# Performance work log

Measured on AMD Instinct MI355X. Metric: run time of the kernel, lower is better.

## Reference

```python
import jax, jax.numpy as jnp
from jax import lax
import numpy as np

B, NR, NC, FEAT = 8, 1024, 1024, 768
N = NR + NC
HID, GATD, GRUD = 256, 128, 64
NEG = -9e15  # matches -9000000000000000.0 in torch source


def setup_inputs() -> dict:
    key = jax.random.key(0)
    ks = jax.random.split(key, 24)
    s = 0.02
    nrm = lambda k, shp: jax.random.normal(k, shp, jnp.float32) * s
    z = lambda shp: jnp.zeros(shp, jnp.float32)
    inp = {}
    inp['req_nodes'] = jax.random.normal(ks[0], (B, NR, FEAT), jnp.float32)
    inp['code_nodes'] = jax.random.normal(ks[1], (B, NC, FEAT), jnp.float32)
    inp['alignment_matrix'] = jax.random.bernoulli(ks[2], 0.05, (B, N, N)).astype(jnp.float32)
    inp['total_nodes'] = jax.random.randint(ks[3], (B,), N // 2, N + 1).astype(jnp.int32)
    # feature_projection
    inp['W_proj'] = nrm(ks[4], (HID, FEAT)); inp['b_proj'] = z((HID,))
    # GAT layer 1 (HID->HID), attention weight a is Linear(2*HID, 1, bias=False)
    inp['W_g1'] = nrm(ks[5], (HID, HID)); inp['b_g1'] = z((HID,)); inp['a_g1'] = nrm(ks[6], (2 * HID,))
    # GAT layer 2 (HID->GATD)
    inp['W_g2'] = nrm(ks[7], (GATD, HID)); inp['b_g2'] = z((GATD,)); inp['a_g2'] = nrm(ks[8], (2 * GATD,))
    # bidirectional GRU (torch layout: [3H, in], gates r|z|n)
    inp['Wih_f'] = nrm(ks[9], (3 * GRUD, GATD)); inp['Whh_f'] = nrm(ks[10], (3 * GRUD, GRUD))
    inp['bih_f'] = z((3 * GRUD,)); inp['bhh_f'] = z((3 * GRUD,))
    inp['Wih_b'] = nrm(ks[11], (3 * GRUD, GATD)); inp['Whh_b'] = nrm(ks[12], (3 * GRUD, GRUD))
    inp['bih_b'] = z((3 * GRUD,)); inp['bhh_b'] = z((3 * GRUD,))
    inp['W_fus'] = nrm(ks[13], (GRUD, 2 * GRUD)); inp['b_fus'] = z((GRUD,))
    inp['W_c1'] = nrm(ks[14], (HID // 2, GRUD)); inp['b_c1'] = z((HID // 2,))
    inp['W_c2'] = nrm(ks[15], (1, HID // 2)); inp['b_c2'] = z((1,))
    return inp


def _gat_layer(x, adj, mask, W, b, a):
    # h: [B, N, D]
    h = x @ W.T + b
    D = h.shape[-1]
    # attention(concat(h_i, h_j)) == a[:D]@h_i + a[D:]@h_j -> never materialize [B,N,N,2D]
    s_src = h @ a[:D]   # [B, N]
    s_dst = h @ a[D:]   # [B, N]
    e = jax.nn.leaky_relu(s_src[:, :, None] + s_dst[:, None, :], 0.01)  # [B,N,N]
    att = jax.nn.softmax(jnp.where(adj > 0, e, NEG), axis=-1)
    out = jnp.einsum('bij,bjd->bid', att, h)
    return out * mask[..., None]


def _gru_dir(xproj, Whh, bhh, reverse):
    # xproj: [B, T, 3H] = x @ Wih.T + bih (precomputed)
    Bv, H = xproj.shape[0], Whh.shape[1]
    def step(h, xt):
        gh = h @ Whh.T + bhh
        ir, iz, inn = jnp.split(xt, 3, axis=-1)
        hr, hz, hn = jnp.split(gh, 3, axis=-1)
        r = jax.nn.sigmoid(ir + hr)
        zt = jax.nn.sigmoid(iz + hz)
        n = jnp.tanh(inn + r * hn)
        hnew = (1.0 - zt) * n + zt * h
        return hnew, hnew
    h0 = jnp.zeros((Bv, H), xproj.dtype)
    _, ys = lax.scan(step, h0, jnp.swapaxes(xproj, 0, 1), reverse=reverse)
    return jnp.swapaxes(ys, 0, 1)  # [B, T, H]


def _forward(req_nodes, code_nodes, alignment_matrix, total_nodes,
             W_proj, b_proj, W_g1, b_g1, a_g1, W_g2, b_g2, a_g2,
             Wih_f, Whh_f, bih_f, bhh_f, Wih_b, Whh_b, bih_b, bhh_b,
             W_fus, b_fus, W_c1, b_c1, W_c2, b_c2):
    x = jnp.concatenate([req_nodes, code_nodes], axis=1)        # [B, N, FEAT]
    proj = jax.nn.relu(x @ W_proj.T + b_proj)                   # dropout is eval-mode identity
    Nt = proj.shape[1]
    mask = (jnp.arange(Nt)[None, :] < total_nodes[:, None]).astype(proj.dtype)  # [B, N]
    g1 = _gat_layer(proj, alignment_matrix, mask, W_g1, b_g1, a_g1)
    g1 = jax.nn.relu(g1) * mask[..., None]
    gat_out = _gat_layer(g1, alignment_matrix, mask, W_g2, b_g2, a_g2)
    gat_out = gat_out * mask[..., None]  # extra masking as in torch source (idempotent)
    gf = _gru_dir(gat_out @ Wih_f.T + bih_f, Whh_f, bhh_f, reverse=False)
    gb = _gru_dir(gat_out @ Wih_b.T + bih_b, Whh_b, bhh_b, reverse=True)
    gru_out = jnp.concatenate([gf, gb], axis=-1) * mask[..., None]  # [B, N, 2*GRUD]
    fused = gru_out @ W_fus.T + b_fus                               # [B, N, GRUD]
    pooled = jnp.mean(fused, axis=1)  # AdaptiveAvgPool1d(1) over seq dim
    h1 = jax.nn.relu(pooled @ W_c1.T + b_c1)
    out = jax.nn.sigmoid(h1 @ W_c2.T + b_c2)  # [B, 1]
    return out


def reference(req_nodes, code_nodes, alignment_matrix, total_nodes,
              W_proj, b_proj, W_g1, b_g1, a_g1, W_g2, b_g2, a_g2,
              Wih_f, Whh_f, bih_f, bhh_f, Wih_b, Whh_b, bih_b, bhh_b,
              W_fus, b_fus, W_c1, b_c1, W_c2, b_c2):
    return _forward(req_nodes, code_nodes, alignment_matrix, total_nodes,
                    W_proj, b_proj, W_g1, b_g1, a_g1, W_g2, b_g2, a_g2,
                    Wih_f, Whh_f, bih_f, bhh_f, Wih_b, Whh_b, bih_b, bhh_b,
                    W_fus, b_fus, W_c1, b_c1, W_c2, b_c2)
```

## Files before the change

### kernel.cpp

```cpp
#include <hip/hip_runtime.h>
#include <stdint.h>

#define EMAX 256

typedef short bf16x8 __attribute__((ext_vector_type(8)));
typedef float f32x4 __attribute__((ext_vector_type(4)));
typedef _Float16 h2_t __attribute__((ext_vector_type(2)));

#define SWZ(r, c) ((r) * 64 + ((c) ^ (((r) & 7) << 3)))

__device__ __forceinline__ uint16_t f2bf(float f) {
    union { float f; uint32_t u; } v; v.f = f;
    uint32_t u = v.u;
    uint32_t r = (u + 0x7FFFu + ((u >> 16) & 1u)) >> 16;
    return (uint16_t)r;
}
__device__ __forceinline__ float bf2f(uint16_t h) {
    union { uint32_t u; float f; } v; v.u = ((uint32_t)h) << 16;
    return v.f;
}
__device__ __forceinline__ h2_t u2h2(uint32_t u) {
    union { uint32_t u; h2_t h; } v; v.u = u;
    return v.h;
}
__device__ __forceinline__ uint32_t cvtpk_bf16(float lo, float hi) {
    uint32_t d;
    asm("v_cvt_pk_bf16_f32 %0, %1, %2" : "=v"(d) : "v"(lo), "v"(hi));
    return d;
}

__global__ __launch_bounds__(256) void k_prep(const float* wp, const float* wg1, const float* wg2,
                                              const float* wif, const float* wib,
                                              const float* whf, const float* whb,
                                              const float* bihf, const float* bihb,
                                              uint16_t* op, uint16_t* og1, uint16_t* og2,
                                              uint16_t* oifb, _Float16* ohf, _Float16* ohb, float* bihfb,
                                              float* __restrict__ Sz) {
    int i = blockIdx.x * 256 + threadIdx.x;
    if (i < 196608) op[i]  = f2bf(wp[i]);
    if (i < 65536)  og1[i] = f2bf(wg1[i]);
    if (i < 32768)  og2[i] = f2bf(wg2[i]);
    if (i < 24576)  { oifb[i] = f2bf(wif[i]); oifb[24576 + i] = f2bf(wib[i]); }
    if (i < 12288)  { ohf[i] = (_Float16)whf[i]; ohb[i] = (_Float16)whb[i]; }
    if (i < 192)    { bihfb[i] = bihf[i]; bihfb[192 + i] = bihb[i]; }
    if (i < 1024)   Sz[i] = 0.f;
}

__global__ __launch_bounds__(256) void k_g1e(const float* __restrict__ req, const float* __restrict__ code,
                                             const uint16_t* __restrict__ Bw,
                                             const float* __restrict__ bias,
                                             uint16_t* __restrict__ C,
                                             const float* __restrict__ adj,
                                             uint16_t* __restrict__ eidx, int* __restrict__ ecnt) {
    __shared__ __align__(16) uint16_t As[64 * 64];
    __shared__ __align__(16) uint16_t Bs[64 * 64];
    int tid = threadIdx.x;
    if (blockIdx.x < 4096) {
        int row  = blockIdx.x * 4 + (tid >> 6);
        int lane = tid & 63;
        const float4* ar4 = (const float4*)(adj + (size_t)row * 2048) + lane;
        float4 vv[8];
#pragma unroll
        for (int c = 0; c < 8; ++c) vv[c] = ar4[c * 64];
        uint32_t m4[8]; int c4[8];
#pragma unroll
        for (int c = 0; c < 8; ++c) {
            uint32_t m = (vv[c].x > 0.f ? 1u : 0u) | (vv[c].y > 0.f ? 2u : 0u)
                       | (vv[c].z > 0.f ? 4u : 0u) | (vv[c].w > 0.f ? 8u : 0u);
            m4[c] = m; c4[c] = __popc(m);
        }
        int pk[4];
#pragma unroll
        for (int q = 0; q < 4; ++q) pk[q] = c4[2 * q] | (c4[2 * q + 1] << 16);
#pragma unroll
        for (int off = 1; off < 64; off <<= 1) {
#pragma unroll
            for (int q = 0; q < 4; ++q) {
                int o = __shfl_up(pk[q], off);
                if (lane >= off) pk[q] += o;
            }
        }
        uint16_t* outr = eidx + (size_t)row * EMAX;
        int base = 0;
#pragma unroll
        for (int c = 0; c < 8; ++c) {
            int incl = (pk[c >> 1] >> ((c & 1) * 16)) & 0xffff;
            int Tc   = __shfl(incl, 63);
            int p    = base + incl - c4[c];
            uint32_t mm = m4[c];
            int cb = c * 256 + lane * 4;
            while (mm) {
                int k = __builtin_ctz(mm);
                mm &= mm - 1u;
                if (p < EMAX) outr[p] = (uint16_t)(cb + k);
                ++p;
            }
            base += Tc;
        }
        if (lane == 0) ecnt[row] = (base < EMAX) ? base : EMAX;
        return;
    }
    constexpr int K = 768, N = 256;
    int g = blockIdx.x - 4096;
    int n0 = (g & 3) * 64, m0 = (g >> 2) * 64;
    int wave = tid >> 6, lane = tid & 63;
    int quad = lane >> 4, l16 = lane & 15;
    f32x4 acc[4] = {};
    int ar = tid >> 3;
    int ac = (tid & 7) * 8;
    const float4* rowp[2];
#pragma unroll
    for (int h = 0; h < 2; ++h) {
        int n = m0 + ar + h * 32;
        int b = n >> 11, n2 = n & 2047;
        const float* s = (n2 < 1024) ? (req  + ((size_t)(b * 1024 + n2)) * 768)
                                     : (code + ((size_t)(b * 1024 + (n2 - 1024))) * 768);
        rowp[h] = (const float4*)s + (ac >> 2);
    }
    for (int kb = 0; kb < K; kb += 64) {
#pragma unroll
        for (int h = 0; h < 2; ++h) {
            float4 f0 = rowp[h][(kb >> 2) + 0];
            float4 f1 = rowp[h][(kb >> 2) + 1];
            uint4 pk;
            pk.x = cvtpk_bf16(f0.x, f0.y); pk.y = cvtpk_bf16(f0.z, f0.w);
            pk.z = cvtpk_bf16(f1.x, f1.y); pk.w = cvtpk_bf16(f1.z, f1.w);
            *(uint4*)&As[SWZ(ar + h * 32, ac)] = pk;
        }
        *(uint4*)&Bs[SWZ(ar, ac)]      = *(const uint4*)(Bw + (size_t)(n0 + ar)      * K + kb + ac);
        *(uint4*)&Bs[SWZ(ar + 32, ac)] = *(const uint4*)(Bw + (size_t)(n0 + ar + 32) * K + kb + ac);
        __syncthreads();
#pragma unroll
        for (int kk = 0; kk < 64; kk += 32) {
            bf16x8 af = *(bf16x8*)&As[SWZ(wave * 16 + l16, kk + quad * 8)];
#pragma unroll
            for (int c = 0; c < 4; ++c) {
                bf16x8 bfr = *(bf16x8*)&Bs[SWZ(c * 16 + l16, kk + quad * 8)];
                acc[c] = __builtin_amdgcn_mfma_f32_16x16x32_bf16(af, bfr, acc[c], 0, 0, 0);
            }
        }
        __syncthreads();
    }
#pragma unroll
    for (int c = 0; c < 4; ++c) {
        int col = n0 + c * 16 + l16;
        float bv = bias[col];
#pragma unroll
        for (int rg = 0; rg < 4; ++rg) {
            int row = m0 + wave * 16 + quad * 4 + rg;
            float v = fmaxf(acc[c][rg] + bv, 0.f);
            C[(size_t)row * N + col] = f2bf(v);
        }
    }
}

template<int ACT, int MODE>
__global__ __launch_bounds__(256) void k_gemm(const uint16_t* __restrict__ A,
                                              const uint16_t* __restrict__ Bw,
                                              const float* __restrict__ bias,
                                              void* __restrict__ Cv, void* __restrict__ Cv2,
                                              int M, int N, int K) {
    __shared__ __align__(16) uint16_t As[64 * 64];
    __shared__ __align__(16) uint16_t Bs[64 * 64];
    int tid = threadIdx.x;
    int n0 = blockIdx.x * 64, m0 = blockIdx.y * 64;
    int wave = tid >> 6, lane = tid & 63;
    int quad = lane >> 4, l16 = lane & 15;
    f32x4 acc[4] = {};
    int ar = tid >> 3;
    int ac = (tid & 7) * 8;
    for (int kb = 0; kb < K; kb += 64) {
        *(uint4*)&As[SWZ(ar, ac)]      = *(const uint4*)(A  + (size_t)(m0 + ar)      * K + kb + ac);
        *(uint4*)&As[SWZ(ar + 32, ac)] = *(const uint4*)(A  + (size_t)(m0 + ar + 32) * K + kb + ac);
        *(uint4*)&Bs[SWZ(ar, ac)]      = *(const uint4*)(Bw + (size_t)(n0 + ar)      * K + kb + ac);
        *(uint4*)&Bs[SWZ(ar + 32, ac)] = *(const uint4*)(Bw + (size_t)(n0 + ar + 32) * K + kb + ac);
        __syncthreads();
#pragma unroll
        for (int kk = 0; kk < 64; kk += 32) {
            bf16x8 af = *(bf16x8*)&As[SWZ(wave * 16 + l16, kk + quad * 8)];
#pragma unroll
            for (int c = 0; c < 4; ++c) {
                bf16x8 bfr = *(bf16x8*)&Bs[SWZ(c * 16 + l16, kk + quad * 8)];
                acc[c] = __builtin_amdgcn_mfma_f32_16x16x32_bf16(af, bfr, acc[c], 0, 0, 0);
            }
        }
        __syncthreads();
    }
#pragma unroll
    for (int c = 0; c < 4; ++c) {
        int col = n0 + c * 16 + l16;
        float bv = bias ? bias[col] : 0.f;
#pragma unroll
        for (int rg = 0; rg < 4; ++rg) {
            int row = m0 + wave * 16 + quad * 4 + rg;
            float v = acc[c][rg] + bv;
            if (ACT == 1) v = fmaxf(v, 0.f);
            if (MODE == 1)      ((uint16_t*)Cv)[(size_t)row * N + col] = f2bf(v);
            else if (MODE == 0) ((float*)Cv)[(size_t)row * N + col] = v;
            else {
                int tc = (col < 192) ? col : col - 192;
                int dc = (tc & 63) * 4 + (tc >> 6);
                float* dst = (col < 192) ? (float*)Cv : (float*)Cv2;
                dst[(size_t)row * 256 + dc] = v;
            }
        }
    }
}

template<int D>
__global__ __launch_bounds__(256) void k_attvec(const uint16_t* __restrict__ H,
                                                const float* __restrict__ a,
                                                float* __restrict__ ssrc,
                                                float* __restrict__ sdst) {
    int row  = blockIdx.x * 4 + (threadIdx.x >> 6);
    int lane = threadIdx.x & 63;
    constexpr int PER = D >> 6;
    const uint32_t* hr = (const uint32_t*)(H + (size_t)row * D + lane * PER);
    float s0 = 0.f, s1 = 0.f;
#pragma unroll
    for (int q = 0; q < PER / 2; ++q) {
        uint32_t hv = hr[q];
        int d = lane * PER + q * 2;
        float h0 = bf2f((uint16_t)hv), h1 = bf2f((uint16_t)(hv >> 16));
        s0 += h0 * a[d] + h1 * a[d + 1];
        s1 += h0 * a[D + d] + h1 * a[D + d + 1];
    }
    for (int off = 32; off; off >>= 1) { s0 += __shfl_down(s0, off); s1 += __shfl_down(s1, off); }
    if (lane == 0) { ssrc[row] = s0; sdst[row] = s1; }
}

#define ACC4(hv, wv) { \
    a0 = fmaf(wv, bf2f((uint16_t)(hv).x), a0); \
    a1 = fmaf(wv, bf2f((uint16_t)((hv).x >> 16)), a1); \
    a2 = fmaf(wv, bf2f((uint16_t)(hv).y), a2); \
    a3 = fmaf(wv, bf2f((uint16_t)((hv).y >> 16)), a3); }

template<int D, int LAYER1>
__global__ __launch_bounds__(256) void k_agg(const uint16_t* __restrict__ H,
                                             const float* __restrict__ ssrc,
                                             const float* __restrict__ sdst,
                                             const uint16_t* __restrict__ eidx,
                                             const int* __restrict__ ecnt,
                                             const int* __restrict__ total,
                                             uint16_t* __restrict__ out) {
    constexpr int LPG = (D == 256) ? 64 : 32;
    constexpr int G   = 64 / LPG;
    constexpr int RS  = D / 4;
    __shared__ __align__(16) uint2 ew[4][EMAX];
    int tid  = threadIdx.x;
    int wid  = tid >> 6, lane = tid & 63;
    int grp  = lane / LPG;
    int c    = lane % LPG;
    int b    = blockIdx.x & 7;
    int i    = ((blockIdx.x >> 3) << 2) + wid;
    int row  = (b << 11) + i;
    uint2* orow = (uint2*)(out + (size_t)row * D);
    if (i >= total[b]) {
        if (grp == 0) { uint2 z; z.x = 0u; z.y = 0u; orow[c] = z; }
        return;
    }
    int cnt = ecnt[row];
    const uint2* H2 = (const uint2*)(H + (size_t)b * 2048 * D);
    float a0 = 0.f, a1 = 0.f, a2 = 0.f, a3 = 0.f;
    if (cnt > 0) {
        float sv = ssrc[row];
        const uint16_t* er = eidx + (size_t)row * EMAX;
        int   jj[4]; float ee[4];
#pragma unroll
        for (int k = 0; k < 4; ++k) {
            int t = lane + 64 * k;
            int j = (t < cnt) ? (int)er[t] : 0;
            float x = sv + sdst[b * 2048 + j];
            float e = (x > 0.f) ? x : 0.01f * x;
            if (t >= cnt) e = -1e30f;
            jj[k] = j; ee[k] = e;
        }
        float m = fmaxf(fmaxf(ee[0], ee[1]), fmaxf(ee[2], ee[3]));
#pragma unroll
        for (int off = 32; off; off >>= 1) m = fmaxf(m, __shfl_xor(m, off));
        float w[4]; float s = 0.f;
#pragma unroll
        for (int k = 0; k < 4; ++k) { w[k] = __expf(ee[k] - m); s += w[k]; }
#pragma unroll
        for (int off = 32; off; off >>= 1) s += __shfl_xor(s, off);
        float inv = 1.f / s;
#pragma unroll
        for (int k = 0; k < 4; ++k) {
            uint2 p; p.x = (uint32_t)jj[k]; p.y = __float_as_uint(w[k] * inv);
            ew[wid][lane + 64 * k] = p;
        }
        asm volatile("s_waitcnt lgkmcnt(0)" ::: "memory");
        constexpr int EPB = 4 * G;
        int cntP = (cnt + EPB - 1) & ~(EPB - 1);
        if constexpr (G == 1) {
            for (int t = 0; t < cntP; t += 4) {
                uint2 e0 = ew[wid][t + 0], e1 = ew[wid][t + 1];
                uint2 e2 = ew[wid][t + 2], e3 = ew[wid][t + 3];
                uint2 h0 = H2[(size_t)e0.x * RS + c];
                uint2 h1 = H2[(size_t)e1.x * RS + c];
                uint2 h2 = H2[(size_t)e2.x * RS + c];
                uint2 h3 = H2[(size_t)e3.x * RS + c];
                ACC4(h0, __uint_as_float(e0.y));
                ACC4(h1, __uint_as_float(e1.y));
                ACC4(h2, __uint_as_float(e2.y));
                ACC4(h3, __uint_as_float(e3.y));
            }
        } else {
            for (int t = 0; t < cntP; t += 8) {
                uint2 e0 = ew[wid][t + 0 + grp], e1 = ew[wid][t + 2 + grp];
                uint2 e2 = ew[wid][t + 4 + grp], e3 = ew[wid][t + 6 + grp];
                uint2 h0 = H2[(size_t)e0.x * RS + c];
                uint2 h1 = H2[(size_t)e1.x * RS + c];
                uint2 h2 = H2[(size_t)e2.x * RS + c];
                uint2 h3 = H2[(size_t)e3.x * RS + c];
                ACC4(h0, __uint_as_float(e0.y));
                ACC4(h1, __uint_as_float(e1.y));
                ACC4(h2, __uint_as_float(e2.y));
                ACC4(h3, __uint_as_float(e3.y));
            }
        }
    } else {
        for (int t = grp; t < 2048; t += G) {
            uint2 hv = H2[(size_t)t * RS + c];
            ACC4(hv, 1.f);
        }
        a0 *= (1.f / 2048.f); a1 *= (1.f / 2048.f);
        a2 *= (1.f / 2048.f); a3 *= (1.f / 2048.f);
    }
    if constexpr (G == 2) {
        a0 += __shfl_xor(a0, 32); a1 += __shfl_xor(a1, 32);
        a2 += __shfl_xor(a2, 32); a3 += __shfl_xor(a3, 32);
    }
    if (LAYER1) {
        a0 = fmaxf(a0, 0.f); a1 = fmaxf(a1, 0.f);
        a2 = fmaxf(a2, 0.f); a3 = fmaxf(a3, 0.f);
    }
    if (grp == 0) {
        uint2 pk;
        pk.x = (uint32_t)f2bf(a0) | ((uint32_t)f2bf(a1) << 16);
        pk.y = (uint32_t)f2bf(a2) | ((uint32_t)f2bf(a3) << 16);
        orow[c] = pk;
    }
}

#define CHUNKS 16
#define CLEN   128
#define WARM   64
#define FDOT2(acc, p, wq) acc = __builtin_amdgcn_fdot2(p, u2h2(wq), acc, false)
#define DOTBLK(hq, q) { \
    h2_t p0 = u2h2(hq.x), p1 = u2h2(hq.y), p2 = u2h2(hq.z), p3 = u2h2(hq.w); \
    FDOT2(ar0, p0, wr[4*q+0]); FDOT2(ar1, p1, wr[4*q+1]); FDOT2(ar2, p2, wr[4*q+2]); FDOT2(ar3, p3, wr[4*q+3]); \
    FDOT2(az0, p0, wz[4*q+0]); FDOT2(az1, p1, wz[4*q+1]); FDOT2(az2, p2, wz[4*q+2]); FDOT2(az3, p3, wz[4*q+3]); \
    FDOT2(an0, p0, wn[4*q+0]); FDOT2(an1, p1, wn[4*q+1]); FDOT2(an2, p2, wn[4*q+2]); FDOT2(an3, p3, wn[4*q+3]); }
#define GRU_STEP(xq) { \
    uint4 h0 = hv4[0], h1 = hv4[1], h2v = hv4[2], h3 = hv4[3]; \
    uint4 h4 = hv4[4], h5 = hv4[5], h6 = hv4[6], h7 = hv4[7]; \
    float ar0 = br, ar1 = 0.f, ar2 = 0.f, ar3 = 0.f; \
    float az0 = bz, az1 = 0.f, az2 = 0.f, az3 = 0.f; \
    float an0 = bn, an1 = 0.f, an2 = 0.f, an3 = 0.f; \
    DOTBLK(h0, 0) DOTBLK(h1, 1) DOTBLK(h2v, 2) DOTBLK(h3, 3) \
    DOTBLK(h4, 4) DOTBLK(h5, 5) DOTBLK(h6, 6) DOTBLK(h7, 7) \
    float ghr = (ar0 + ar1) + (ar2 + ar3); \
    float ghz = (az0 + az1) + (az2 + az3); \
    float ghn = (an0 + an1) + (an2 + an3); \
    float er = __expf(-(xq.x + ghr)); \
    float r = __builtin_amdgcn_rcpf(1.f + er); \
    float ez = __expf(-(xq.y + ghz)); \
    float z = __builtin_amdgcn_rcpf(1.f + ez); \
    float nv = fmaf(r, ghn, xq.z); \
    float en = __expf(-2.f * nv); \
    float n = fmaf(-2.f, __builtin_amdgcn_rcpf(1.f + en), 1.f); \
    hj = fmaf(z, hj - n, n); \
    sj += (t < Tcur) ? hj : 0.f; \
    hb[j] = (_Float16)hj; \
    asm volatile("" ::: "memory"); \
    t += dt; }

__global__ __attribute__((amdgpu_flat_work_group_size(64, 64), amdgpu_waves_per_eu(1, 1)))
void k_gru(const float* __restrict__ XPf, const float* __restrict__ XPb,
           const _Float16* __restrict__ WhF, const _Float16* __restrict__ WhB,
           const float* __restrict__ bhh_f, const float* __restrict__ bhh_b,
           const int* __restrict__ total,
           float* __restrict__ S) {
    int blk   = blockIdx.x;
    int chunk = blk & (CHUNKS - 1);
    int sc    = blk >> 4;
    int dir   = sc >> 3;
    int b     = sc & 7;
    int j     = threadIdx.x;
    const float* XP  = dir ? XPb : XPf;
    const uint32_t* Wd = (const uint32_t*)(dir ? WhB : WhF);
    const float* bhh = dir ? bhh_b : bhh_f;
    uint32_t wr[32], wz[32], wn[32];
#pragma unroll
    for (int c = 0; c < 32; ++c) {
        wr[c] = Wd[(size_t)(      j) * 32 + c];
        wz[c] = Wd[(size_t)( 64 + j) * 32 + c];
        wn[c] = Wd[(size_t)(128 + j) * 32 + c];
    }
    float br = bhh[j], bz = bhh[64 + j], bn = bhh[128 + j];
    __shared__ __align__(16) _Float16 hbuf[64];
    _Float16* hb = hbuf;
    hb[j] = (_Float16)0.f;
    asm volatile("s_waitcnt lgkmcnt(0)" ::: "memory");
    float hj = 0.f, sj = 0.f;
    int Tb = total[b];
    int s0 = chunk * CLEN - WARM;
    int W0 = WARM;
    if (s0 < 0) { s0 = 0; W0 = 0; }
    const float4* xbase = (const float4*)(XP + (size_t)b * 2048 * 256) + j;
    int xstep = dir ? -64 : 64;
    const float4* xptr = xbase + (size_t)(dir ? (2047 - s0) : s0) * 64;
    float4 x0 = *xptr; xptr += xstep;
    float4 x1 = *xptr; xptr += xstep;
    float4 x2 = *xptr; xptr += xstep;
    float4 x3 = *xptr; xptr += xstep;
    int t = dir ? (2047 - s0) : s0, dt = dir ? -1 : 1;
    const uint4* hv4 = (const uint4*)hb;
    int Tcur = -1;
    for (int su = 0; su < W0; su += 4) {
        GRU_STEP(x0) x0 = *xptr; xptr += xstep;
        GRU_STEP(x1) x1 = *xptr; xptr += xstep;
        GRU_STEP(x2) x2 = *xptr; xptr += xstep;
        GRU_STEP(x3) x3 = *xptr; xptr += xstep;
    }
    Tcur = Tb;
    for (int su = 0; su < CLEN; su += 4) {
        GRU_STEP(x0) x0 = *xptr; xptr += xstep;
        GRU_STEP(x1) x1 = *xptr; xptr += xstep;
        GRU_STEP(x2) x2 = *xptr; xptr += xstep;
        GRU_STEP(x3) x3 = *xptr; xptr += xstep;
    }
    atomicAdd(&S[b * 128 + dir * 64 + j], sj);
}

__global__ __launch_bounds__(128) void k_final(const float* __restrict__ S,
                                               const float* __restrict__ Wfus, const float* __restrict__ bfus,
                                               const float* __restrict__ Wc1, const float* __restrict__ bc1,
                                               const float* __restrict__ Wc2, const float* __restrict__ bc2,
                                               float* __restrict__ out) {
    __shared__ float pool[64];
    __shared__ float red[128];
    int tid = threadIdx.x;
    for (int b = 0; b < 8; ++b) {
        if (tid < 64) {
            float a = 0.f;
            for (int jj = 0; jj < 128; ++jj) a += S[b * 128 + jj] * Wfus[tid * 128 + jj];
            pool[tid] = bfus[tid] + a * (1.f / 2048.f);
        }
        __syncthreads();
        float a1 = 0.f;
        for (int d = 0; d < 64; ++d) a1 += pool[d] * Wc1[tid * 64 + d];
        float h = fmaxf(a1 + bc1[tid], 0.f);
        red[tid] = h * Wc2[tid];
        __syncthreads();
        for (int s = 64; s; s >>= 1) { if (tid < s) red[tid] += red[tid + s]; __syncthreads(); }
        if (tid == 0) out[b] = 1.f / (1.f + __expf(-(red[0] + bc2[0])));
        __syncthreads();
    }
}

extern "C" void kernel_launch(void* const* d_in, const int* in_sizes, int n_in,
                              void* d_out, int out_size, void* d_ws, size_t ws_size,
                              hipStream_t stream) {
    (void)in_sizes; (void)n_in; (void)out_size; (void)ws_size;
    const float* req   = (const float*)d_in[0];
    const float* code  = (const float*)d_in[1];
    const float* adj   = (const float*)d_in[2];
    const int*   total = (const int*)  d_in[3];
    const float* W_proj = (const float*)d_in[4];
    const float* b_proj = (const float*)d_in[5];
    const float* W_g1   = (const float*)d_in[6];
    const float* b_g1   = (const float*)d_in[7];
    const float* a_g1   = (const float*)d_in[8];
    const float* W_g2   = (const float*)d_in[9];
    const float* b_g2   = (const float*)d_in[10];
    const float* a_g2   = (const float*)d_in[11];
    const float* Wih_f  = (const float*)d_in[12];
    const float* Whh_f  = (const float*)d_in[13];
    const float* bih_f  = (const float*)d_in[14];
    const float* bhh_f  = (const float*)d_in[15];
    const float* Wih_b  = (const float*)d_in[16];
    const float* Whh_b  = (const float*)d_in[17];
    const float* bih_b  = (const float*)d_in[18];
    const float* bhh_b  = (const float*)d_in[19];
    const float* W_fus  = (const float*)d_in[20];
    const float* b_fus  = (const float*)d_in[21];
    const float* W_c1   = (const float*)d_in[22];
    const float* b_c1   = (const float*)d_in[23];
    const float* W_c2   = (const float*)d_in[24];
    const float* b_c2   = (const float*)d_in[25];

    char* ws = (char*)d_ws;
    float*    XPf  = (float*)(ws + 4096);
    float*    XPb  = (float*)(ws + 4096 + 16777216 + 4096);
    uint16_t* EIDX = (uint16_t*)(ws + 25169920);
    uint16_t* WPb  = (uint16_t*)(ws + 33570816);
    uint16_t* WG1b = (uint16_t*)(ws + 33964032);
    uint16_t* WG2b = (uint16_t*)(ws + 34095104);
    uint16_t* WIFB = (uint16_t*)(ws + 34160640);
    uint16_t* Pbf  = (uint16_t*)(ws + 34262016);
    uint16_t* H1bf = (uint16_t*)(ws + 42650624);
    uint16_t* H2bf = (uint16_t*)(ws + 42650624);
    uint16_t* G2bf = (uint16_t*)(ws + 46844928);
    uint16_t* G1bf = (uint16_t*)(ws + 51039232);
    int*      ECNT = (int*)     (ws + 59427840);
    float* s1src = (float*)(ws + 59493376);
    float* s1dst = (float*)(ws + 59558912);
    float* s2src = (float*)(ws + 59624448);
    float* s2dst = (float*)(ws + 59689984);
    float* Sbuf  = (float*)(ws + 59755520);
    _Float16* WhFh = (_Float16*)(ws + 59759616);
    _Float16* WhBh = (_Float16*)(ws + 59784192);
    float* BIHFB   = (float*)(ws + 59808768);

    k_prep<<<768, 256, 0, stream>>>(W_proj, W_g1, W_g2, Wih_f, Wih_b, Whh_f, Whh_b, bih_f, bih_b,
                                    WPb, WG1b, WG2b, WIFB, WhFh, WhBh, BIHFB, Sbuf);

    k_g1e<<<5120, 256, 0, stream>>>(req, code, WPb, b_proj, Pbf, adj, EIDX, ECNT);

    k_gemm<0, 1><<<dim3(4, 256), 256, 0, stream>>>(Pbf, WG1b, b_g1, H1bf, nullptr, 16384, 256, 256);
    k_attvec<256><<<4096, 256, 0, stream>>>(H1bf, a_g1, s1src, s1dst);
    k_agg<256, 1><<<4096, 256, 0, stream>>>(H1bf, s1src, s1dst, EIDX, ECNT, total, G1bf);

    k_gemm<0, 1><<<dim3(2, 256), 256, 0, stream>>>(G1bf, WG2b, b_g2, H2bf, nullptr, 16384, 128, 256);
    k_attvec<128><<<4096, 256, 0, stream>>>(H2bf, a_g2, s2src, s2dst);
    k_agg<128, 0><<<4096, 256, 0, stream>>>(H2bf, s2src, s2dst, EIDX, ECNT, total, G2bf);

    k_gemm<0, 2><<<dim3(6, 256), 256, 0, stream>>>(G2bf, WIFB, BIHFB, XPf, XPb, 16384, 384, 128);

    k_gru<<<256, 64, 0, stream>>>(XPf, XPb, WhFh, WhBh, bhh_f, bhh_b, total, Sbuf);

    k_final<<<1, 128, 0, stream>>>(Sbuf, W_fus, b_fus, W_c1, b_c1, W_c2, b_c2, (float*)d_out);
}
```

Baseline: 538.5 us.

## Process multiple adjacency rows per wave with double-buffered loads in edge extraction

The edge-list extraction part of the fused kernel now launches 512 blocks instead of 4096. Each wave handles 8 adjacency rows strided by 2048, loading the next row into a second register buffer while compacting the current one. This is meant to overlap global-memory latency with the scan work and cut block launch overhead. It raises register pressure and lowers the number of waves in flight for the memory-bound scan.

```diff
diff --git a/kernel.cpp b/kernel.cpp
--- a/kernel.cpp
+++ b/kernel.cpp
@@ -55,53 +55,54 @@
     __shared__ __align__(16) uint16_t As[64 * 64];
     __shared__ __align__(16) uint16_t Bs[64 * 64];
     int tid = threadIdx.x;
-    if (blockIdx.x < 4096) {
-        int row  = blockIdx.x * 4 + (tid >> 6);
-        int lane = tid & 63;
-        const float4* ar4 = (const float4*)(adj + (size_t)row * 2048) + lane;
-        float4 vv[8];
-#pragma unroll
-        for (int c = 0; c < 8; ++c) vv[c] = ar4[c * 64];
-        uint32_t m4[8]; int c4[8];
-#pragma unroll
-        for (int c = 0; c < 8; ++c) {
-            uint32_t m = (vv[c].x > 0.f ? 1u : 0u) | (vv[c].y > 0.f ? 2u : 0u)
-                       | (vv[c].z > 0.f ? 4u : 0u) | (vv[c].w > 0.f ? 8u : 0u);
-            m4[c] = m; c4[c] = __popc(m);
-        }
-        int pk[4];
-#pragma unroll
-        for (int q = 0; q < 4; ++q) pk[q] = c4[2 * q] | (c4[2 * q + 1] << 16);
-#pragma unroll
-        for (int off = 1; off < 64; off <<= 1) {
-#pragma unroll
-            for (int q = 0; q < 4; ++q) {
-                int o = __shfl_up(pk[q], off);
-                if (lane >= off) pk[q] += o;
-            }
-        }
-        uint16_t* outr = eidx + (size_t)row * EMAX;
-        int base = 0;
-#pragma unroll
-        for (int c = 0; c < 8; ++c) {
-            int incl = (pk[c >> 1] >> ((c & 1) * 16)) & 0xffff;
-            int Tc   = __shfl(incl, 63);
-            int p    = base + incl - c4[c];
-            uint32_t mm = m4[c];
-            int cb = c * 256 + lane * 4;
-            while (mm) {
-                int k = __builtin_ctz(mm);
-                mm &= mm - 1u;
-                if (p < EMAX) outr[p] = (uint16_t)(cb + k);
-                ++p;
-            }
-            base += Tc;
-        }
-        if (lane == 0) ecnt[row] = (base < EMAX) ? base : EMAX;
+    if (blockIdx.x < 512) {
+        int wid  = tid >> 6, lane = tid & 63;
+        int gw   = blockIdx.x * 4 + wid;
+        const float4* base = (const float4*)adj + lane;
+        float4 va[8], vb[8];
+#define LOADROW(dst, r) { const float4* p_ = base + (size_t)(r) * 512; \
+        _Pragma("unroll") for (int c_ = 0; c_ < 8; ++c_) dst[c_] = p_[c_ * 64]; }
+#define PROCROW(src, r) { \
+        uint32_t m4[8]; int c4[8]; \
+        _Pragma("unroll") for (int c_ = 0; c_ < 8; ++c_) { \
+            uint32_t m_ = (src[c_].x > 0.f ? 1u : 0u) | (src[c_].y > 0.f ? 2u : 0u) \
+                        | (src[c_].z > 0.f ? 4u : 0u) | (src[c_].w > 0.f ? 8u : 0u); \
+            m4[c_] = m_; c4[c_] = __popc(m_); } \
+        int pk[4]; \
+        _Pragma("unroll") for (int q_ = 0; q_ < 4; ++q_) pk[q_] = c4[2*q_] | (c4[2*q_+1] << 16); \
+        _Pragma("unroll") for (int off_ = 1; off_ < 64; off_ <<= 1) { \
+            _Pragma("unroll") for (int q_ = 0; q_ < 4; ++q_) { \
+                int o_ = __shfl_up(pk[q_], off_); \
+                if (lane >= off_) pk[q_] += o_; } } \
+        uint16_t* outr = eidx + (size_t)(r) * EMAX; \
+        int bse = 0; \
+        _Pragma("unroll") for (int c_ = 0; c_ < 8; ++c_) { \
+            int incl = (pk[c_ >> 1] >> ((c_ & 1) * 16)) & 0xffff; \
+            int Tc_  = __shfl(incl, 63); \
+            int p_   = bse + incl - c4[c_]; \
+            uint32_t mm = m4[c_]; \
+            int cb = c_ * 256 + lane * 4; \
+            while (mm) { int k_ = __builtin_ctz(mm); mm &= mm - 1u; \
+                if (p_ < EMAX) outr[p_] = (uint16_t)(cb + k_); ++p_; } \
+            bse += Tc_; } \
+        if (lane == 0) ecnt[r] = (bse < EMAX) ? bse : EMAX; }
+
+        LOADROW(va, gw)
+#pragma unroll
+        for (int it = 0; it < 4; ++it) {
+            int rA = gw + (2 * it) * 2048;
+            int rB = rA + 2048;
+            LOADROW(vb, rB)
+            PROCROW(va, rA)
+            if (it < 3) LOADROW(va, rB + 2048)
+            PROCROW(vb, rB)
+        }
+#undef LOADROW
+#undef PROCROW
         return;
     }
     constexpr int K = 768, N = 256;
-    int g = blockIdx.x - 4096;
+    int g = blockIdx.x - 512;
     int n0 = (g & 3) * 64, m0 = (g >> 2) * 64;
     int wave = tid >> 6, lane = tid & 63;
     int quad = lane >> 4, l16 = lane & 15;
@@ -517,7 +518,7 @@
     k_prep<<<768, 256, 0, stream>>>(W_proj, W_g1, W_g2, Wih_f, Wih_b, Whh_f, Whh_b, bih_f, bih_b,
                                     WPb, WG1b, WG2b, WIFB, WhFh, WhBh, BIHFB, Sbuf);
 
-    k_g1e<<<5120, 256, 0, stream>>>(req, code, WPb, b_proj, Pbf, adj, EIDX, ECNT);
+    k_g1e<<<1536, 256, 0, stream>>>(req, code, WPb, b_proj, Pbf, adj, EIDX, ECNT);
 
     k_gemm<0, 1><<<dim3(4, 256), 256, 0, stream>>>(Pbf, WG1b, b_g1, H1bf, nullptr, 16384, 256, 256);
     k_attvec<256><<<4096, 256, 0, stream>>>(H1bf, a_g1, s1src, s1dst);
```

Measured after the change: 531.2 us. No clear change (-1.4%).
